# Optimization experiments

Measured on AMD Instinct MI355X. Metric: run time of the kernel, lower is better.

## Reference

```python
import jax, jax.numpy as jnp
import numpy as np

NEG_SLOPE = 0.2


def gat_conv(x, src, dst, W, a_src, a_dst, b, heads, out_ch, concat):
    """PyG-style GATConv (eval mode, self-loops already appended to src/dst)."""
    N = x.shape[0]
    h = (x @ W).reshape(N, heads, out_ch)            # [N,H,C]
    alpha_s = jnp.einsum('nhc,hc->nh', h, a_src)     # [N,H]
    alpha_d = jnp.einsum('nhc,hc->nh', h, a_dst)
    e = jax.nn.leaky_relu(alpha_s[src] + alpha_d[dst], NEG_SLOPE)  # [E,H]
    # segment softmax over incoming edges per destination node
    m = jax.ops.segment_max(e, dst, num_segments=N)  # every node has a self loop
    ex = jnp.exp(e - m[dst])
    denom = jax.ops.segment_sum(ex, dst, num_segments=N)
    alpha = ex / (denom[dst] + 1e-16)                # [E,H]
    msg = h[src] * alpha[:, :, None]                 # [E,H,C]
    out = jax.ops.segment_sum(msg, dst, num_segments=N)  # [N,H,C]
    if concat:
        out = out.reshape(N, heads * out_ch)
    else:
        out = out.mean(axis=1)
    return out + b


def setup_inputs() -> dict:
    key = jax.random.key(0)
    ks = jax.random.split(key, 12)
    N, E, F_IN = 100000, 3200000, 512
    H1, C1 = 8, 8           # conv1: heads=8, out=8, concat -> 64
    H2, C2 = 8, 16          # conv2: heads=8, out=num_classes=16, mean over heads
    x = jax.random.normal(ks[0], (N, F_IN), dtype=jnp.float32)
    edge_index = jax.random.randint(ks[1], (2, E), 0, N, dtype=jnp.int32)
    g = lambda k, s, fan: jax.random.normal(k, s, dtype=jnp.float32) / np.sqrt(fan)
    return {
        'x': x,
        'edge_index': edge_index,
        'W1': g(ks[2], (F_IN, H1 * C1), F_IN),
        'a_src1': g(ks[3], (H1, C1), C1),
        'a_dst1': g(ks[4], (H1, C1), C1),
        'b1': jnp.zeros((H1 * C1,), jnp.float32),
        'W2': g(ks[5], (H1 * C1, H2 * C2), H1 * C1),
        'a_src2': g(ks[6], (H2, C2), C2),
        'a_dst2': g(ks[7], (H2, C2), C2),
        'b2': jnp.zeros((C2,), jnp.float32),
    }


def reference(x, edge_index, W1, a_src1, a_dst1, b1, W2, a_src2, a_dst2, b2):
    N = x.shape[0]
    loops = jnp.arange(N, dtype=edge_index.dtype)
    src = jnp.concatenate([edge_index[0], loops])
    dst = jnp.concatenate([edge_index[1], loops])
    h = gat_conv(x, src, dst, W1, a_src1, a_dst1, b1, heads=8, out_ch=8, concat=True)
    h = jax.nn.elu(h)
    out = gat_conv(h, src, dst, W2, a_src2, a_dst2, b2, heads=8, out_ch=16, concat=False)
    return out
```

## Files before the change

kernel.cpp:

```cpp
#include <hip/hip_runtime.h>
#include <hip/hip_bf16.h>
#include <hip/hip_fp16.h>
#include <cstddef>

#define NEG_SLOPE 0.2f

typedef _Float16 half8 __attribute__((ext_vector_type(8)));
typedef float floatx4 __attribute__((ext_vector_type(4)));
typedef float floatx2 __attribute__((ext_vector_type(2)));


__global__ __launch_bounds__(256) void pre_k(const int* __restrict__ dst, int E,
                                             int* __restrict__ bhist, int NB,
                                             const float* __restrict__ W1, _Float16* __restrict__ W1T,
                                             const float* __restrict__ W2, _Float16* __restrict__ W2T) {
    int b = blockIdx.x;
    if (b < 512) {
        __shared__ int lh[256];
        for (int t = threadIdx.x; t < 256; t += 256) lh[t] = 0;
        __syncthreads();
        int per = (E + 511) / 512;
        int s = b * per;
        int e = min(s + per, E);
        for (int i = s + threadIdx.x; i < e; i += 256) atomicAdd(&lh[dst[i] >> 9], 1);
        __syncthreads();
        for (int t = threadIdx.x; t < NB; t += 256)
            if (lh[t]) atomicAdd(&bhist[t], lh[t]);
    } else if (b < 640) {
        int i = (b - 512) * 256 + threadIdx.x;
        if (i < 512 * 64) {
            int k = i / 64, n = i % 64;
            W1T[(size_t)n * 512 + k] = (_Float16)W1[i];
        }
    } else {
        int i = (b - 640) * 256 + threadIdx.x;
        if (i < 64 * 128) {
            int k = i / 128, n = i % 128;
            W2T[(size_t)n * 64 + k] = (_Float16)W2[i];
        }
    }
}

__global__ __launch_bounds__(256) void bucket_scan_k(const int* __restrict__ bhist, int NB,
                                                     int* __restrict__ bbase, int* __restrict__ cursor,
                                                     int* __restrict__ row_start, int N, int E) {
    __shared__ int tmp[256];
    int tid = threadIdx.x;
    int v = (tid < NB) ? bhist[tid] : 0;
    tmp[tid] = v;
    __syncthreads();
    for (int d = 1; d < 256; d <<= 1) {
        int t = tmp[tid];
        int a = (tid >= d) ? tmp[tid - d] : 0;
        __syncthreads();
        tmp[tid] = t + a;
        __syncthreads();
    }
    if (tid < NB) {
        int b = tmp[tid] - v;
        bbase[tid] = b;
        cursor[tid] = b;
    }
    if (tid == 0) {
        bbase[NB] = E;
        row_start[N] = E;
    }
}

__global__ __launch_bounds__(512) void bucket_build_k(const unsigned int* __restrict__ part,
                                                      const int* __restrict__ bbase,
                                                      int* __restrict__ row_start,
                                                      int* __restrict__ csr, int N) {
    __shared__ int cnt[512];
    __shared__ int cur[512];
    int b = blockIdx.x, tid = threadIdx.x;
    int n0 = b << 9;
    int s = bbase[b], e2 = bbase[b + 1];
    cnt[tid] = 0;
    __syncthreads();
    for (int i = s + tid; i < e2; i += 512) atomicAdd(&cnt[part[i] & 511], 1);
    __syncthreads();
    int v = cnt[tid];
    for (int d = 1; d < 512; d <<= 1) {
        int t = cnt[tid];
        int a = (tid >= d) ? cnt[tid - d] : 0;
        __syncthreads();
        cnt[tid] = t + a;
        __syncthreads();
    }
    int excl = cnt[tid] - v;
    if (n0 + tid < N) row_start[n0 + tid] = s + excl;
    cur[tid] = excl;
    __syncthreads();
    for (int i = s + tid; i < e2; i += 512) {
        unsigned u = part[i];
        int p = atomicAdd(&cur[u & 511], 1);
        csr[s + p] = (int)(u >> 9);
    }
}


__global__ __launch_bounds__(256) void gemm1_part_k(
    const float* __restrict__ A, const _Float16* __restrict__ BT,
    const float* __restrict__ a_s, const float* __restrict__ a_d,
    __half* __restrict__ C, float* __restrict__ os, float* __restrict__ od, int M,
    const int* __restrict__ src, const int* __restrict__ dst, int E,
    int* __restrict__ cursor, unsigned int* __restrict__ part, int NB) {
    if (blockIdx.x < 512) {
        __shared__ int lh[256];
        __shared__ int lbase[256];
        for (int t = threadIdx.x; t < 256; t += 256) lh[t] = 0;
        __syncthreads();
        int per = (E + 511) / 512;
        int s = blockIdx.x * per;
        int e = min(s + per, E);
        for (int i = s + threadIdx.x; i < e; i += 256) atomicAdd(&lh[dst[i] >> 9], 1);
        __syncthreads();
        for (int t = threadIdx.x; t < NB; t += 256) {
            int c = lh[t];
            lbase[t] = c ? atomicAdd(&cursor[t], c) : 0;
            lh[t] = 0;
        }
        __syncthreads();
        for (int i = s + threadIdx.x; i < e; i += 256) {
            int d = dst[i];
            int b = d >> 9;
            int lo = atomicAdd(&lh[b], 1);
            part[lbase[b] + lo] = ((unsigned)src[i] << 9) | (unsigned)(d & 511);
        }
        return;
    }
    constexpr int NT = 4, K = 512, Nc = 64;
    int bid = blockIdx.x - 512;
    int wave = threadIdx.x >> 6, lane = threadIdx.x & 63;
    int m16 = lane & 15, quad = lane >> 4;
    int arow = bid * 64 + wave * 16 + m16;
    int arc = arow < M ? arow : M - 1;
    floatx4 acc[NT] = {};
    for (int k0 = 0; k0 < K; k0 += 32) {
        const float* ap = A + (size_t)arc * K + k0 + quad * 8;
        float4 v0 = *(const float4*)ap;
        float4 v1 = *(const float4*)(ap + 4);
        half8 af;
        af[0] = (_Float16)v0.x; af[1] = (_Float16)v0.y;
        af[2] = (_Float16)v0.z; af[3] = (_Float16)v0.w;
        af[4] = (_Float16)v1.x; af[5] = (_Float16)v1.y;
        af[6] = (_Float16)v1.z; af[7] = (_Float16)v1.w;
#pragma unroll
        for (int t = 0; t < NT; ++t) {
            half8 bf = *(const half8*)(BT + (size_t)(t * 16 + m16) * K + k0 + quad * 8);
            acc[t] = __builtin_amdgcn_mfma_f32_16x16x32_f16(af, bf, acc[t], 0, 0, 0);
        }
    }
    int gm0 = bid * 64 + wave * 16 + quad * 4;
    int head = (m16 >> 3);
#pragma unroll
    for (int t = 0; t < NT; ++t) {
        float ws = a_s[(2 * t + head) * 8 + (m16 & 7)];
        float wd = a_d[(2 * t + head) * 8 + (m16 & 7)];
#pragma unroll
        for (int r = 0; r < 4; ++r) {
            int gm = gm0 + r;
            float v = acc[t][r];
            if (gm < M) C[(size_t)gm * Nc + t * 16 + m16] = __float2half(v);
            float s = v * ws, d = v * wd;
            s += __shfl_xor(s, 1, 64); d += __shfl_xor(d, 1, 64);
            s += __shfl_xor(s, 2, 64); d += __shfl_xor(d, 2, 64);
            s += __shfl_xor(s, 4, 64); d += __shfl_xor(d, 4, 64);
            if ((m16 & 7) == 0 && gm < M) {
                os[gm * 8 + 2 * t + head] = s;
                od[gm * 8 + 2 * t + head] = d;
            }
        }
    }
}


__global__ __launch_bounds__(256) void gemm2_k(const _Float16* __restrict__ A,
                                               const _Float16* __restrict__ BT,
                                               const float* __restrict__ a_s,
                                               const float* __restrict__ a_d,
                                               unsigned short* __restrict__ Cf8,
                                               float* __restrict__ os,
                                               float* __restrict__ od, int M) {
    constexpr int NT = 8, K = 64;
    int wave = threadIdx.x >> 6, lane = threadIdx.x & 63;
    int m16 = lane & 15, quad = lane >> 4;
    int arow = blockIdx.x * 64 + wave * 16 + m16;
    int arc = arow < M ? arow : M - 1;
    floatx4 acc[NT] = {};
    for (int k0 = 0; k0 < K; k0 += 32) {
        half8 af = *(const half8*)(A + (size_t)arc * K + k0 + quad * 8);
#pragma unroll
        for (int t = 0; t < NT; ++t) {
            half8 bf = *(const half8*)(BT + (size_t)(t * 16 + m16) * K + k0 + quad * 8);
            acc[t] = __builtin_amdgcn_mfma_f32_16x16x32_f16(af, bf, acc[t], 0, 0, 0);
        }
    }
    int gm0 = blockIdx.x * 64 + wave * 16 + quad * 4;
#pragma unroll
    for (int t = 0; t < NT; ++t) {
        float ws = a_s[t * 16 + m16];
        float wd = a_d[t * 16 + m16];
#pragma unroll
        for (int r = 0; r < 4; ++r) {
            int gm = gm0 + r;
            float v = acc[t][r];
            float o = __shfl_xor(v, 1, 64);
            if (gm < M && !(m16 & 1)) {
                unsigned p = __builtin_amdgcn_cvt_pk_fp8_f32(v, o, 0, false);
                Cf8[(size_t)gm * 64 + t * 8 + (m16 >> 1)] = (unsigned short)(p & 0xffff);
            }
            float s = v * ws, d = v * wd;
            s += __shfl_xor(s, 1, 64); d += __shfl_xor(d, 1, 64);
            s += __shfl_xor(s, 2, 64); d += __shfl_xor(d, 2, 64);
            s += __shfl_xor(s, 4, 64); d += __shfl_xor(d, 4, 64);
            s += __shfl_xor(s, 8, 64); d += __shfl_xor(d, 8, 64);
            if (gm < M && m16 == t) {
                os[gm * 8 + t] = s;
                od[gm * 8 + t] = d;
            }
        }
    }
}


__global__ __launch_bounds__(256) void aggregate1_k(
    const uint2* __restrict__ H1, const float* __restrict__ as,
    const float* __restrict__ ad, const int* __restrict__ row_start,
    const int* __restrict__ csr, const float* __restrict__ b1,
    uint2* __restrict__ h1o, int N) {
    int l = threadIdx.x & 63;
    int wv = threadIdx.x >> 6;
    int ll = l & 31;
    int n = min((int)(blockIdx.x * 8 + wv * 2 + (l >> 5)), N - 1);
    int k = ll & 15;
    int jj = ll >> 4;
    int h = k >> 1;

    float adv = ad[n * 8 + h];
    float e0 = as[n * 8 + h] + adv;
    e0 = fmaxf(e0, NEG_SLOPE * e0);
    float ex0 = __expf(e0);
    float x0 = jj ? 0.f : ex0;

    uint2 sv = H1[(size_t)n * 16 + k];
    float2 s01 = __half22float2(*(const __half2*)&sv.x);
    float2 s23 = __half22float2(*(const __half2*)&sv.y);
    float denom = x0;
    float a0 = x0 * s01.x, a1 = x0 * s01.y, a2 = x0 * s23.x, a3 = x0 * s23.y;

    int e = row_start[n], end = row_start[n + 1];
    for (; e + 8 <= end; e += 8) {
#pragma unroll
        for (int u = 0; u < 4; ++u) {
            int sj = csr[e + 2 * u + jj];
            float t = as[sj * 8 + h] + adv;
            t = fmaxf(t, NEG_SLOPE * t);
            float x = __expf(t);
            uint2 gv = H1[(size_t)sj * 16 + k];
            float2 v01 = __half22float2(*(const __half2*)&gv.x);
            float2 v23 = __half22float2(*(const __half2*)&gv.y);
            denom += x;
            a0 = fmaf(x, v01.x, a0); a1 = fmaf(x, v01.y, a1);
            a2 = fmaf(x, v23.x, a2); a3 = fmaf(x, v23.y, a3);
        }
    }
    if (e < end) {
#pragma unroll
        for (int u = 0; u < 4; ++u) {
            int idx = e + 2 * u + jj;
            int sj = csr[min(idx, end - 1)];
            float t = as[sj * 8 + h] + adv;
            t = fmaxf(t, NEG_SLOPE * t);
            float x = idx < end ? __expf(t) : 0.f;
            uint2 gv = H1[(size_t)sj * 16 + k];
            float2 v01 = __half22float2(*(const __half2*)&gv.x);
            float2 v23 = __half22float2(*(const __half2*)&gv.y);
            denom += x;
            a0 = fmaf(x, v01.x, a0); a1 = fmaf(x, v01.y, a1);
            a2 = fmaf(x, v23.x, a2); a3 = fmaf(x, v23.y, a3);
        }
    }
    denom += __shfl_xor(denom, 16, 64);
    a0 += __shfl_xor(a0, 16, 64);
    a1 += __shfl_xor(a1, 16, 64);
    a2 += __shfl_xor(a2, 16, 64);
    a3 += __shfl_xor(a3, 16, 64);
    float inv = 1.f / denom;
    float r0 = a0 * inv + b1[4 * k + 0];
    float r1 = a1 * inv + b1[4 * k + 1];
    float r2 = a2 * inv + b1[4 * k + 2];
    float r3 = a3 * inv + b1[4 * k + 3];
    r0 = r0 > 0.f ? r0 : expm1f(r0);
    r1 = r1 > 0.f ? r1 : expm1f(r1);
    r2 = r2 > 0.f ? r2 : expm1f(r2);
    r3 = r3 > 0.f ? r3 : expm1f(r3);
    if (!jj) {
        __half2 p01 = __floats2half2_rn(r0, r1);
        __half2 p23 = __floats2half2_rn(r2, r3);
        uint2 o;
        o.x = *(const unsigned*)&p01;
        o.y = *(const unsigned*)&p23;
        h1o[(size_t)n * 16 + k] = o;
    }
}


__global__ __launch_bounds__(256) void aggregate2_k(
    const uint2* __restrict__ H2, const float* __restrict__ as,
    const float* __restrict__ ad, const int* __restrict__ row_start,
    const int* __restrict__ csr, const float* __restrict__ b2,
    float* __restrict__ out, int N) {
    int l = threadIdx.x & 63;
    int wv = threadIdx.x >> 6;
    int ll = l & 31;
    int n = min((int)(blockIdx.x * 8 + wv * 2 + (l >> 5)), N - 1);
    int k = ll & 15;
    int jj = ll >> 4;
    int h = k >> 1;

    float adv = ad[n * 8 + h];
    float e0 = as[n * 8 + h] + adv;
    e0 = fmaxf(e0, NEG_SLOPE * e0);
    float ex0 = __expf(e0);
    float x0 = jj ? 0.f : ex0;

    uint2 sv = H2[(size_t)n * 16 + k];
    floatx2 p01 = __builtin_amdgcn_cvt_pk_f32_fp8((int)sv.x, false);
    floatx2 p23 = __builtin_amdgcn_cvt_pk_f32_fp8((int)sv.x, true);
    floatx2 p45 = __builtin_amdgcn_cvt_pk_f32_fp8((int)sv.y, false);
    floatx2 p67 = __builtin_amdgcn_cvt_pk_f32_fp8((int)sv.y, true);
    float denom = x0;
    float a0 = x0 * p01[0], a1 = x0 * p01[1], a2 = x0 * p23[0], a3 = x0 * p23[1];
    float a4 = x0 * p45[0], a5 = x0 * p45[1], a6 = x0 * p67[0], a7 = x0 * p67[1];

    int e = row_start[n], end = row_start[n + 1];
    for (; e + 8 <= end; e += 8) {
#pragma unroll
        for (int u = 0; u < 4; ++u) {
            int sj = csr[e + 2 * u + jj];
            float t = as[sj * 8 + h] + adv;
            t = fmaxf(t, NEG_SLOPE * t);
            float x = __expf(t);
            uint2 gv = H2[(size_t)sj * 16 + k];
            floatx2 v01 = __builtin_amdgcn_cvt_pk_f32_fp8((int)gv.x, false);
            floatx2 v23 = __builtin_amdgcn_cvt_pk_f32_fp8((int)gv.x, true);
            floatx2 v45 = __builtin_amdgcn_cvt_pk_f32_fp8((int)gv.y, false);
            floatx2 v67 = __builtin_amdgcn_cvt_pk_f32_fp8((int)gv.y, true);
            denom += x;
            a0 = fmaf(x, v01[0], a0); a1 = fmaf(x, v01[1], a1);
            a2 = fmaf(x, v23[0], a2); a3 = fmaf(x, v23[1], a3);
            a4 = fmaf(x, v45[0], a4); a5 = fmaf(x, v45[1], a5);
            a6 = fmaf(x, v67[0], a6); a7 = fmaf(x, v67[1], a7);
        }
    }
    if (e < end) {
#pragma unroll
        for (int u = 0; u < 4; ++u) {
            int idx = e + 2 * u + jj;
            int sj = csr[min(idx, end - 1)];
            float t = as[sj * 8 + h] + adv;
            t = fmaxf(t, NEG_SLOPE * t);
            float x = idx < end ? __expf(t) : 0.f;
            uint2 gv = H2[(size_t)sj * 16 + k];
            floatx2 v01 = __builtin_amdgcn_cvt_pk_f32_fp8((int)gv.x, false);
            floatx2 v23 = __builtin_amdgcn_cvt_pk_f32_fp8((int)gv.x, true);
            floatx2 v45 = __builtin_amdgcn_cvt_pk_f32_fp8((int)gv.y, false);
            floatx2 v67 = __builtin_amdgcn_cvt_pk_f32_fp8((int)gv.y, true);
            denom += x;
            a0 = fmaf(x, v01[0], a0); a1 = fmaf(x, v01[1], a1);
            a2 = fmaf(x, v23[0], a2); a3 = fmaf(x, v23[1], a3);
            a4 = fmaf(x, v45[0], a4); a5 = fmaf(x, v45[1], a5);
            a6 = fmaf(x, v67[0], a6); a7 = fmaf(x, v67[1], a7);
        }
    }
    denom += __shfl_xor(denom, 16, 64);
    float inv = 1.f / denom;
    a0 *= inv; a1 *= inv; a2 *= inv; a3 *= inv;
    a4 *= inv; a5 *= inv; a6 *= inv; a7 *= inv;
#pragma unroll
    for (int m = 2; m <= 16; m <<= 1) {
        a0 += __shfl_xor(a0, m, 64);
        a1 += __shfl_xor(a1, m, 64);
        a2 += __shfl_xor(a2, m, 64);
        a3 += __shfl_xor(a3, m, 64);
        a4 += __shfl_xor(a4, m, 64);
        a5 += __shfl_xor(a5, m, 64);
        a6 += __shfl_xor(a6, m, 64);
        a7 += __shfl_xor(a7, m, 64);
    }
    if (ll < 2) {
        int c0 = k * 8;
        float4 o0, o1;
        o0.x = a0 * 0.125f + b2[c0 + 0];
        o0.y = a1 * 0.125f + b2[c0 + 1];
        o0.z = a2 * 0.125f + b2[c0 + 2];
        o0.w = a3 * 0.125f + b2[c0 + 3];
        o1.x = a4 * 0.125f + b2[c0 + 4];
        o1.y = a5 * 0.125f + b2[c0 + 5];
        o1.z = a6 * 0.125f + b2[c0 + 6];
        o1.w = a7 * 0.125f + b2[c0 + 7];
        *(float4*)(out + (size_t)n * 16 + c0) = o0;
        *(float4*)(out + (size_t)n * 16 + c0 + 4) = o1;
    }
}


extern "C" void kernel_launch(void* const* d_in, const int* in_sizes, int n_in,
                              void* d_out, int out_size, void* d_ws, size_t ws_size,
                              hipStream_t stream) {
    (void)n_in; (void)out_size; (void)ws_size;
    const float* x      = (const float*)d_in[0];
    const int*   ei     = (const int*)d_in[1];
    const float* W1     = (const float*)d_in[2];
    const float* a_src1 = (const float*)d_in[3];
    const float* a_dst1 = (const float*)d_in[4];
    const float* b1     = (const float*)d_in[5];
    const float* W2     = (const float*)d_in[6];
    const float* a_src2 = (const float*)d_in[7];
    const float* a_dst2 = (const float*)d_in[8];
    const float* b2     = (const float*)d_in[9];

    int N = in_sizes[0] / 512;
    int E = in_sizes[1] / 2;
    const int* src = ei;
    const int* dst = ei + E;
    int NB = (N + 511) >> 9;

    char* ws = (char*)d_ws;
    size_t off = 0;
    auto alloc = [&](size_t bytes) -> void* {
        void* p = ws + off;
        off = (off + bytes + 255) & ~(size_t)255;
        return p;
    };
    __half* h1  = (__half*)alloc((size_t)N * 64 * 2);
    __half* h1o = (__half*)alloc((size_t)N * 64 * 2);
    unsigned short* h2f8 = (unsigned short*)alloc((size_t)N * 64 * 2);
    float* as1  = (float*)alloc((size_t)N * 8 * 4);
    float* ad1  = (float*)alloc((size_t)N * 8 * 4);
    float* as2  = (float*)alloc((size_t)N * 8 * 4);
    float* ad2  = (float*)alloc((size_t)N * 8 * 4);
    _Float16* W1T = (_Float16*)alloc((size_t)512 * 64 * 2);
    _Float16* W2T = (_Float16*)alloc((size_t)64 * 128 * 2);
    int* row_start = (int*)alloc((size_t)(N + 1) * 4);
    int* bhist     = (int*)alloc(256 * 4);
    int* bbase     = (int*)alloc(257 * 4);
    int* cursor    = (int*)alloc(256 * 4);
    unsigned int* part = (unsigned int*)alloc((size_t)E * 4);
    int* csr       = (int*)alloc((size_t)E * 4);

    hipMemsetAsync(bhist, 0, 256 * 4, stream);
    pre_k<<<672, 256, 0, stream>>>(dst, E, bhist, NB, W1, W1T, W2, W2T);
    bucket_scan_k<<<1, 256, 0, stream>>>(bhist, NB, bbase, cursor, row_start, N, E);

    int gblocks = (N + 63) / 64;
    int ablocks = (N + 7) / 8;

    gemm1_part_k<<<512 + gblocks, 256, 0, stream>>>(x, W1T, a_src1, a_dst1, h1, as1, ad1, N,
                                                    src, dst, E, cursor, part, NB);
    bucket_build_k<<<NB, 512, 0, stream>>>(part, bbase, row_start, csr, N);

    aggregate1_k<<<ablocks, 256, 0, stream>>>((const uint2*)h1, as1, ad1, row_start,
                                              csr, b1, (uint2*)h1o, N);

    gemm2_k<<<gblocks, 256, 0, stream>>>((const _Float16*)h1o, W2T, a_src2, a_dst2,
                                         h2f8, as2, ad2, N);
    aggregate2_k<<<ablocks, 256, 0, stream>>>((const uint2*)h2f8, as2, ad2,
                                              row_start, csr, b2, (float*)d_out, N);
}
```

Measured before the change: 643.8 us.

## Split partition from GEMM1, add LDS-tiled GEMM1 and deeper aggregation unroll

The edge partitioning is unfused from the first GEMM. Per-block bucket histograms are now saved and column-scanned, so each block gets deterministic write offsets instead of claiming them through atomic cursor adds. GEMM1 becomes its own kernel with 128-row tiles, a double-buffered swizzled LDS copy of W1T, and register prefetch of the next A chunk. Both aggregation kernels gain a 16-edge unrolled loop that batches index loads and exps, exposing more memory-level parallelism. This adds two small launches and loses the overlap between partitioning and the GEMM.

```diff
diff --git a/kernel.cpp b/kernel.cpp
--- a/kernel.cpp
+++ b/kernel.cpp
@@ -11,7 +11,8 @@
 
 
 __global__ __launch_bounds__(256) void pre_k(const int* __restrict__ dst, int E,
-                                             int* __restrict__ bhist, int NB,
+                                             int* __restrict__ bhist, int* __restrict__ bh_blocks,
+                                             int NB,
                                              const float* __restrict__ W1, _Float16* __restrict__ W1T,
                                              const float* __restrict__ W2, _Float16* __restrict__ W2T) {
     int b = blockIdx.x;
@@ -24,8 +25,11 @@
         int e = min(s + per, E);
         for (int i = s + threadIdx.x; i < e; i += 256) atomicAdd(&lh[dst[i] >> 9], 1);
         __syncthreads();
-        for (int t = threadIdx.x; t < NB; t += 256)
-            if (lh[t]) atomicAdd(&bhist[t], lh[t]);
+        for (int t = threadIdx.x; t < 256; t += 256) {
+            int c = lh[t];
+            bh_blocks[b * 256 + t] = c;
+            if (c && t < NB) atomicAdd(&bhist[t], c);
+        }
     } else if (b < 640) {
         int i = (b - 512) * 256 + threadIdx.x;
         if (i < 512 * 64) {
@@ -42,7 +46,7 @@
 }
 
 __global__ __launch_bounds__(256) void bucket_scan_k(const int* __restrict__ bhist, int NB,
-                                                     int* __restrict__ bbase, int* __restrict__ cursor,
+                                                     int* __restrict__ bbase,
                                                      int* __restrict__ row_start, int N, int E) {
     __shared__ int tmp[256];
     int tid = threadIdx.x;
@@ -57,13 +61,57 @@
         __syncthreads();
     }
     if (tid < NB) {
-        int b = tmp[tid] - v;
-        bbase[tid] = b;
-        cursor[tid] = b;
+        bbase[tid] = tmp[tid] - v;
     }
     if (tid == 0) {
         bbase[NB] = E;
         row_start[N] = E;
+    }
+}
+
+__global__ __launch_bounds__(256) void colscan_k(const int* __restrict__ bh_blocks,
+                                                 const int* __restrict__ bbase,
+                                                 int* __restrict__ pbase) {
+    __shared__ int ssum[256];
+    int t = blockIdx.x;
+    int i = threadIdx.x;
+    int v0 = bh_blocks[(2 * i) * 256 + t];
+    int v1 = bh_blocks[(2 * i + 1) * 256 + t];
+    int s = v0 + v1;
+    ssum[i] = s;
+    __syncthreads();
+    for (int d = 1; d < 256; d <<= 1) {
+        int x = ssum[i];
+        int a = (i >= d) ? ssum[i - d] : 0;
+        __syncthreads();
+        ssum[i] = x + a;
+        __syncthreads();
+    }
+    int excl = ssum[i] - s + bbase[t];
+    pbase[(2 * i) * 256 + t] = excl;
+    pbase[(2 * i + 1) * 256 + t] = excl + v0;
+}
+
+__global__ __launch_bounds__(256) void partition_k(const int* __restrict__ src,
+                                                   const int* __restrict__ dst, int E,
+                                                   const int* __restrict__ pbase,
+                                                   unsigned int* __restrict__ part) {
+    __shared__ int lbase[256];
+    __shared__ int lh[256];
+    int b = blockIdx.x;
+    for (int t = threadIdx.x; t < 256; t += 256) {
+        lbase[t] = pbase[b * 256 + t];
+        lh[t] = 0;
+    }
+    __syncthreads();
+    int per = (E + 511) / 512;
+    int s = b * per;
+    int e = min(s + per, E);
+    for (int i = s + threadIdx.x; i < e; i += 256) {
+        int d = dst[i];
+        int bk = d >> 9;
+        int lo = atomicAdd(&lh[bk], 1);
+        part[lbase[bk] + lo] = ((unsigned)src[i] << 9) | (unsigned)(d & 511);
     }
 }
 
@@ -100,76 +148,119 @@
 }
 
 
-__global__ __launch_bounds__(256) void gemm1_part_k(
-    const float* __restrict__ A, const _Float16* __restrict__ BT,
-    const float* __restrict__ a_s, const float* __restrict__ a_d,
-    __half* __restrict__ C, float* __restrict__ os, float* __restrict__ od, int M,
-    const int* __restrict__ src, const int* __restrict__ dst, int E,
-    int* __restrict__ cursor, unsigned int* __restrict__ part, int NB) {
-    if (blockIdx.x < 512) {
-        __shared__ int lh[256];
-        __shared__ int lbase[256];
-        for (int t = threadIdx.x; t < 256; t += 256) lh[t] = 0;
-        __syncthreads();
-        int per = (E + 511) / 512;
-        int s = blockIdx.x * per;
-        int e = min(s + per, E);
-        for (int i = s + threadIdx.x; i < e; i += 256) atomicAdd(&lh[dst[i] >> 9], 1);
-        __syncthreads();
-        for (int t = threadIdx.x; t < NB; t += 256) {
-            int c = lh[t];
-            lbase[t] = c ? atomicAdd(&cursor[t], c) : 0;
-            lh[t] = 0;
-        }
-        __syncthreads();
-        for (int i = s + threadIdx.x; i < e; i += 256) {
-            int d = dst[i];
-            int b = d >> 9;
-            int lo = atomicAdd(&lh[b], 1);
-            part[lbase[b] + lo] = ((unsigned)src[i] << 9) | (unsigned)(d & 511);
-        }
-        return;
-    }
-    constexpr int NT = 4, K = 512, Nc = 64;
-    int bid = blockIdx.x - 512;
-    int wave = threadIdx.x >> 6, lane = threadIdx.x & 63;
+__global__ __launch_bounds__(256) void gemm1_k(const float* __restrict__ A,
+                                               const _Float16* __restrict__ BT,
+                                               const float* __restrict__ a_s,
+                                               const float* __restrict__ a_d,
+                                               __half* __restrict__ C,
+                                               float* __restrict__ os,
+                                               float* __restrict__ od, int M) {
+    constexpr int K = 512;
+    __shared__ __align__(16) _Float16 Bs[2][64 * 64];
+    int tid = threadIdx.x;
+    int wave = tid >> 6, lane = tid & 63;
     int m16 = lane & 15, quad = lane >> 4;
-    int arow = bid * 64 + wave * 16 + m16;
-    int arc = arow < M ? arow : M - 1;
-    floatx4 acc[NT] = {};
-    for (int k0 = 0; k0 < K; k0 += 32) {
-        const float* ap = A + (size_t)arc * K + k0 + quad * 8;
-        float4 v0 = *(const float4*)ap;
-        float4 v1 = *(const float4*)(ap + 4);
-        half8 af;
-        af[0] = (_Float16)v0.x; af[1] = (_Float16)v0.y;
-        af[2] = (_Float16)v0.z; af[3] = (_Float16)v0.w;
-        af[4] = (_Float16)v1.x; af[5] = (_Float16)v1.y;
-        af[6] = (_Float16)v1.z; af[7] = (_Float16)v1.w;
-#pragma unroll
-        for (int t = 0; t < NT; ++t) {
-            half8 bf = *(const half8*)(BT + (size_t)(t * 16 + m16) * K + k0 + quad * 8);
-            acc[t] = __builtin_amdgcn_mfma_f32_16x16x32_f16(af, bf, acc[t], 0, 0, 0);
-        }
-    }
-    int gm0 = bid * 64 + wave * 16 + quad * 4;
+    int row0 = blockIdx.x * 128 + wave * 32;
+    int r0 = min(row0 + m16, M - 1);
+    int r1 = min(row0 + 16 + m16, M - 1);
+    const float* a0p = A + (size_t)r0 * K + quad * 8;
+    const float* a1p = A + (size_t)r1 * K + quad * 8;
+
+    int brow = tid >> 2;
+    int bcb = tid & 3;
+    const _Float16* bsrc = BT + (size_t)brow * K + bcb * 16;
+    int du0 = ((bcb * 2 + 0) * 8) ^ ((brow & 7) << 3);
+    int du1 = ((bcb * 2 + 1) * 8) ^ ((brow & 7) << 3);
+    int dbase = brow * 64;
+
+    floatx4 acc[2][4] = {};
+    half8 b0 = *(const half8*)(bsrc + 0);
+    half8 b1 = *(const half8*)(bsrc + 8);
+    float4 a00 = *(const float4*)(a0p + 0);
+    float4 a01 = *(const float4*)(a0p + 4);
+    float4 a02 = *(const float4*)(a0p + 32);
+    float4 a03 = *(const float4*)(a0p + 36);
+    float4 a10 = *(const float4*)(a1p + 0);
+    float4 a11 = *(const float4*)(a1p + 4);
+    float4 a12 = *(const float4*)(a1p + 32);
+    float4 a13 = *(const float4*)(a1p + 36);
+    *(half8*)(&Bs[0][0] + dbase + du0) = b0;
+    *(half8*)(&Bs[0][0] + dbase + du1) = b1;
+    __syncthreads();
+
+    int cur = 0;
+    for (int s = 0; s < 8; ++s) {
+        half8 af[2][2];
+        af[0][0][0] = (_Float16)a00.x; af[0][0][1] = (_Float16)a00.y;
+        af[0][0][2] = (_Float16)a00.z; af[0][0][3] = (_Float16)a00.w;
+        af[0][0][4] = (_Float16)a01.x; af[0][0][5] = (_Float16)a01.y;
+        af[0][0][6] = (_Float16)a01.z; af[0][0][7] = (_Float16)a01.w;
+        af[0][1][0] = (_Float16)a02.x; af[0][1][1] = (_Float16)a02.y;
+        af[0][1][2] = (_Float16)a02.z; af[0][1][3] = (_Float16)a02.w;
+        af[0][1][4] = (_Float16)a03.x; af[0][1][5] = (_Float16)a03.y;
+        af[0][1][6] = (_Float16)a03.z; af[0][1][7] = (_Float16)a03.w;
+        af[1][0][0] = (_Float16)a10.x; af[1][0][1] = (_Float16)a10.y;
+        af[1][0][2] = (_Float16)a10.z; af[1][0][3] = (_Float16)a10.w;
+        af[1][0][4] = (_Float16)a11.x; af[1][0][5] = (_Float16)a11.y;
+        af[1][0][6] = (_Float16)a11.z; af[1][0][7] = (_Float16)a11.w;
+        af[1][1][0] = (_Float16)a12.x; af[1][1][1] = (_Float16)a12.y;
+        af[1][1][2] = (_Float16)a12.z; af[1][1][3] = (_Float16)a12.w;
+        af[1][1][4] = (_Float16)a13.x; af[1][1][5] = (_Float16)a13.y;
+        af[1][1][6] = (_Float16)a13.z; af[1][1][7] = (_Float16)a13.w;
+        if (s < 7) {
+            int k1 = (s + 1) * 64;
+            b0 = *(const half8*)(bsrc + k1);
+            b1 = *(const half8*)(bsrc + k1 + 8);
+            a00 = *(const float4*)(a0p + k1);
+            a01 = *(const float4*)(a0p + k1 + 4);
+            a02 = *(const float4*)(a0p + k1 + 32);
+            a03 = *(const float4*)(a0p + k1 + 36);
+            a10 = *(const float4*)(a1p + k1);
+            a11 = *(const float4*)(a1p + k1 + 4);
+            a12 = *(const float4*)(a1p + k1 + 32);
+            a13 = *(const float4*)(a1p + k1 + 36);
+        }
+        const _Float16* bsC = &Bs[cur][0];
+#pragma unroll
+        for (int t = 0; t < 4; ++t) {
+#pragma unroll
+            for (int kk = 0; kk < 2; ++kk) {
+                int idx = (t * 16 + m16) * 64 + ((kk * 32 + quad * 8) ^ ((m16 & 7) << 3));
+                half8 bf = *(const half8*)(bsC + idx);
+                acc[0][t] = __builtin_amdgcn_mfma_f32_16x16x32_f16(af[0][kk], bf, acc[0][t], 0, 0, 0);
+                acc[1][t] = __builtin_amdgcn_mfma_f32_16x16x32_f16(af[1][kk], bf, acc[1][t], 0, 0, 0);
+            }
+        }
+        if (s < 7) {
+            _Float16* bsN = &Bs[cur ^ 1][0];
+            *(half8*)(bsN + dbase + du0) = b0;
+            *(half8*)(bsN + dbase + du1) = b1;
+        }
+        __syncthreads();
+        cur ^= 1;
+    }
+
     int head = (m16 >> 3);
 #pragma unroll
-    for (int t = 0; t < NT; ++t) {
-        float ws = a_s[(2 * t + head) * 8 + (m16 & 7)];
-        float wd = a_d[(2 * t + head) * 8 + (m16 & 7)];
-#pragma unroll
-        for (int r = 0; r < 4; ++r) {
-            int gm = gm0 + r;
-            float v = acc[t][r];
-            if (gm < M) C[(size_t)gm * Nc + t * 16 + m16] = __float2half(v);
-            float s = v * ws, d = v * wd;
-            s += __shfl_xor(s, 1, 64); d += __shfl_xor(d, 1, 64);
-            s += __shfl_xor(s, 2, 64); d += __shfl_xor(d, 2, 64);
-            s += __shfl_xor(s, 4, 64); d += __shfl_xor(d, 4, 64);
-            if ((m16 & 7) == 0 && gm < M) {
-                os[gm * 8 + 2 * t + head] = s;
-                od[gm * 8 + 2 * t + head] = d;
+    for (int rt = 0; rt < 2; ++rt) {
+        int gmb = row0 + rt * 16 + quad * 4;
+#pragma unroll
+        for (int t = 0; t < 4; ++t) {
+            float ws = a_s[(2 * t + head) * 8 + (m16 & 7)];
+            float wd = a_d[(2 * t + head) * 8 + (m16 & 7)];
+#pragma unroll
+            for (int r = 0; r < 4; ++r) {
+                int gm = gmb + r;
+                float v = acc[rt][t][r];
+                if (gm < M) C[(size_t)gm * 64 + t * 16 + m16] = __float2half(v);
+                float sv = v * ws, dv = v * wd;
+                sv += __shfl_xor(sv, 1, 64); dv += __shfl_xor(dv, 1, 64);
+                sv += __shfl_xor(sv, 2, 64); dv += __shfl_xor(dv, 2, 64);
+                sv += __shfl_xor(sv, 4, 64); dv += __shfl_xor(dv, 4, 64);
+                if ((m16 & 7) == 0 && gm < M) {
+                    os[gm * 8 + 2 * t + head] = sv;
+                    od[gm * 8 + 2 * t + head] = dv;
+                }
             }
         }
     }
@@ -251,6 +342,27 @@
     float a0 = x0 * s01.x, a1 = x0 * s01.y, a2 = x0 * s23.x, a3 = x0 * s23.y;
 
     int e = row_start[n], end = row_start[n + 1];
+    for (; e + 16 <= end; e += 16) {
+        int sj[8];
+        float xv[8];
+#pragma unroll
+        for (int u = 0; u < 8; ++u) sj[u] = csr[e + 2 * u + jj];
+#pragma unroll
+        for (int u = 0; u < 8; ++u) {
+            float t = as[sj[u] * 8 + h] + adv;
+            t = fmaxf(t, NEG_SLOPE * t);
+            xv[u] = __expf(t);
+        }
+#pragma unroll
+        for (int u = 0; u < 8; ++u) {
+            uint2 gv = H1[(size_t)sj[u] * 16 + k];
+            float2 v01 = __half22float2(*(const __half2*)&gv.x);
+            float2 v23 = __half22float2(*(const __half2*)&gv.y);
+            denom += xv[u];
+            a0 = fmaf(xv[u], v01.x, a0); a1 = fmaf(xv[u], v01.y, a1);
+            a2 = fmaf(xv[u], v23.x, a2); a3 = fmaf(xv[u], v23.y, a3);
+        }
+    }
     for (; e + 8 <= end; e += 8) {
 #pragma unroll
         for (int u = 0; u < 4; ++u) {
@@ -336,6 +448,32 @@
     float a4 = x0 * p45[0], a5 = x0 * p45[1], a6 = x0 * p67[0], a7 = x0 * p67[1];
 
     int e = row_start[n], end = row_start[n + 1];
+    for (; e + 16 <= end; e += 16) {
+        int sj[8];
+        float xv[8];
+#pragma unroll
+        for (int u = 0; u < 8; ++u) sj[u] = csr[e + 2 * u + jj];
+#pragma unroll
+        for (int u = 0; u < 8; ++u) {
+            float t = as[sj[u] * 8 + h] + adv;
+            t = fmaxf(t, NEG_SLOPE * t);
+            xv[u] = __expf(t);
+        }
+#pragma unroll
+        for (int u = 0; u < 8; ++u) {
+            uint2 gv = H2[(size_t)sj[u] * 16 + k];
+            floatx2 v01 = __builtin_amdgcn_cvt_pk_f32_fp8((int)gv.x, false);
+            floatx2 v23 = __builtin_amdgcn_cvt_pk_f32_fp8((int)gv.x, true);
+            floatx2 v45 = __builtin_amdgcn_cvt_pk_f32_fp8((int)gv.y, false);
+            floatx2 v67 = __builtin_amdgcn_cvt_pk_f32_fp8((int)gv.y, true);
+            float x = xv[u];
+            denom += x;
+            a0 = fmaf(x, v01[0], a0); a1 = fmaf(x, v01[1], a1);
+            a2 = fmaf(x, v23[0], a2); a3 = fmaf(x, v23[1], a3);
+            a4 = fmaf(x, v45[0], a4); a5 = fmaf(x, v45[1], a5);
+            a6 = fmaf(x, v67[0], a6); a7 = fmaf(x, v67[1], a7);
+        }
+    }
     for (; e + 8 <= end; e += 8) {
 #pragma unroll
         for (int u = 0; u < 4; ++u) {
@@ -447,26 +585,28 @@
     int* row_start = (int*)alloc((size_t)(N + 1) * 4);
     int* bhist     = (int*)alloc(256 * 4);
     int* bbase     = (int*)alloc(257 * 4);
-    int* cursor    = (int*)alloc(256 * 4);
+    int* bh_blocks = (int*)alloc((size_t)512 * 256 * 4);
+    int* pbase     = (int*)alloc((size_t)512 * 256 * 4);
     unsigned int* part = (unsigned int*)alloc((size_t)E * 4);
     int* csr       = (int*)alloc((size_t)E * 4);
 
     hipMemsetAsync(bhist, 0, 256 * 4, stream);
-    pre_k<<<672, 256, 0, stream>>>(dst, E, bhist, NB, W1, W1T, W2, W2T);
-    bucket_scan_k<<<1, 256, 0, stream>>>(bhist, NB, bbase, cursor, row_start, N, E);
-
-    int gblocks = (N + 63) / 64;
-    int ablocks = (N + 7) / 8;
-
-    gemm1_part_k<<<512 + gblocks, 256, 0, stream>>>(x, W1T, a_src1, a_dst1, h1, as1, ad1, N,
-                                                    src, dst, E, cursor, part, NB);
+    pre_k<<<672, 256, 0, stream>>>(dst, E, bhist, bh_blocks, NB, W1, W1T, W2, W2T);
+    bucket_scan_k<<<1, 256, 0, stream>>>(bhist, NB, bbase, row_start, N, E);
+    colscan_k<<<NB, 256, 0, stream>>>(bh_blocks, bbase, pbase);
+    partition_k<<<512, 256, 0, stream>>>(src, dst, E, pbase, part);
     bucket_build_k<<<NB, 512, 0, stream>>>(part, bbase, row_start, csr, N);
 
+    int g1blocks = (N + 127) / 128;
+    int g2blocks = (N + 63) / 64;
+    int ablocks  = (N + 7) / 8;
+
+    gemm1_k<<<g1blocks, 256, 0, stream>>>(x, W1T, a_src1, a_dst1, h1, as1, ad1, N);
     aggregate1_k<<<ablocks, 256, 0, stream>>>((const uint2*)h1, as1, ad1, row_start,
                                               csr, b1, (uint2*)h1o, N);
 
-    gemm2_k<<<gblocks, 256, 0, stream>>>((const _Float16*)h1o, W2T, a_src2, a_dst2,
-                                         h2f8, as2, ad2, N);
+    gemm2_k<<<g2blocks, 256, 0, stream>>>((const _Float16*)h1o, W2T, a_src2, a_dst2,
+                                          h2f8, as2, ad2, N);
     aggregate2_k<<<ablocks, 256, 0, stream>>>((const uint2*)h2f8, as2, ad2,
                                               row_start, csr, b2, (float*)d_out, N);
 }
```

After: 626.8 us. -2.6%, faster.
